# Optimization experiments

Measured on AMD Instinct MI355X. Metric: run time of the kernel, lower is better.

The kernel has to match this reference:

```python
import jax, jax.numpy as jnp
import numpy as np

N_NODES = 50000
N_EDGES = 800000
D = 128


def sage_conv(x, src, dst, w_nbr, w_root, b, n_nodes):
    # mean aggregation of neighbor features: messages flow src (j) -> dst (i)
    msg_sum = jax.ops.segment_sum(x[src], dst, num_segments=n_nodes)  # [N, D]
    deg = jax.ops.segment_sum(jnp.ones((src.shape[0],), x.dtype), dst,
                              num_segments=n_nodes)
    mean = msg_sum / jnp.maximum(deg, 1.0)[:, None]
    # PyG SAGEConv: lin_l(aggr) + lin_r(x); bias lives in lin_l
    return mean @ w_nbr + x @ w_root + b


def setup_inputs() -> dict:
    key = jax.random.key(0)
    ks = jax.random.split(key, 16)
    s = 1.0 / np.sqrt(D)
    inp = {
        "x": jax.random.normal(ks[0], (N_NODES, D), jnp.float32),
        "edge_index": jax.random.randint(ks[1], (2, N_EDGES), 0, N_NODES,
                                         dtype=jnp.int64),
    }
    for l in range(3):
        inp[f"w_nbr{l}"] = jax.random.normal(ks[2 + 3 * l], (D, D), jnp.float32) * s
        inp[f"w_root{l}"] = jax.random.normal(ks[3 + 3 * l], (D, D), jnp.float32) * s
        inp[f"b{l}"] = jnp.zeros((D,), jnp.float32)
    inp["w_cls"] = jax.random.normal(ks[12], (D, 1), jnp.float32) * s
    inp["b_cls"] = jnp.zeros((1,), jnp.float32)
    return inp


def reference(x, edge_index, w_nbr0, w_root0, b0, w_nbr1, w_root1, b1,
              w_nbr2, w_root2, b2, w_cls, b_cls):
    src, dst = edge_index[0], edge_index[1]
    n = x.shape[0]
    layers = [(w_nbr0, w_root0, b0), (w_nbr1, w_root1, b1), (w_nbr2, w_root2, b2)]
    h = x
    for i, (wn, wr, b) in enumerate(layers):
        h = sage_conv(h, src, dst, wn, wr, b, n)
        if i < len(layers) - 1:
            h = jax.nn.relu(h)  # dropout is identity in eval mode
    return (h @ w_cls + b_cls).squeeze(-1)  # [N]
```

## Files before the change

kernel.cpp:

```cpp
#include <hip/hip_runtime.h>

#define N_NODES 50000
#define N_EDGES 800000
#define D 128
#define NGROUPS 3125
#define NBUK 256
#define NPB 196
#define EPB 2048
#define NBLK 391
#define LTOT (NBUK * NBLK)
#define NSCB 98

typedef __attribute__((ext_vector_type(8))) short short8;
typedef __attribute__((ext_vector_type(4))) float f32x4;

__device__ __forceinline__ float bits2f(unsigned int u) {
    union { unsigned int u; float f; } c; c.u = u; return c.f;
}
__device__ __forceinline__ unsigned short f2b(float f) {
    union { float f; unsigned int u; } c; c.f = f;
    unsigned int r = c.u + 0x7fffu + ((c.u >> 16) & 1u);
    return (unsigned short)(r >> 16);
}


__global__ __launch_bounds__(256) void k_big(
    const int* __restrict__ dst, int* __restrict__ cnt,
    const float* __restrict__ x,
    const float* __restrict__ wn0, const float* __restrict__ wr0,
    const float* __restrict__ wn1, const float* __restrict__ wr1,
    const float* __restrict__ wn2, const float* __restrict__ wr2,
    const float* __restrict__ b2, const float* __restrict__ wc,
    const float* __restrict__ bc,
    unsigned short* __restrict__ f0, unsigned short* __restrict__ f1,
    unsigned short* __restrict__ f2, unsigned short* __restrict__ Bp,
    float* __restrict__ uvc) {
    __shared__ int lc[NBUK];
    int b = blockIdx.x;
    int tid = threadIdx.x;
    if (b < NBLK) {
        lc[tid] = 0;
        __syncthreads();
        #pragma unroll
        for (int k = 0; k < 8; ++k) {
            int e = b * EPB + k * 256 + tid;
            if (e < N_EDGES) atomicAdd(&lc[dst[e] / NPB], 1);
        }
        __syncthreads();
        cnt[b * NBUK + tid] = lc[tid];
    } else if (b < 6641) {
        int i = (b - NBLK) * 256 + tid;
        float4 v = reinterpret_cast<const float4*>(x)[i];
        ushort4 o;
        o.x = f2b(v.x); o.y = f2b(v.y); o.z = f2b(v.z); o.w = f2b(v.w);
        reinterpret_cast<ushort4*>(f0)[i] = o;
    } else if (b < 6673) {
        int t = (b - 6641) * 256 + tid;
        int layer = t >> 12;
        int rem = t & 4095;
        int kstep = rem >> 9;
        int cf = (rem >> 6) & 7;
        int lane = t & 63;
        const float* W = (kstep < 4) ? (layer ? wn1 : wn0) : (layer ? wr1 : wr0);
        int kb = kstep * 32 + (lane >> 4) * 8;
        int colv = cf * 16 + (lane & 15);
        int koff = (kstep < 4) ? kb : kb - 128;
        unsigned short* dstp = Bp + (((layer * 64 + kstep * 8 + cf) * 64 + lane) << 3);
        #pragma unroll
        for (int i = 0; i < 8; ++i) dstp[i] = f2b(W[(koff + i) * D + colv]);
    } else if (b == 6673) {
        if (tid < D) {
            f0[(size_t)N_NODES * D + tid] = 0;
            f1[(size_t)N_NODES * D + tid] = 0;
            f2[(size_t)N_NODES * D + tid] = 0;
        }
    } else {
        if (tid < 128) {
            float su = 0.f;
            for (int m = 0; m < 128; ++m) su += wn2[tid * D + m] * wc[m];
            uvc[tid] = su;
        } else {
            int k = tid - 128;
            float sv = 0.f;
            for (int m = 0; m < 128; ++m) sv += wr2[k * D + m] * wc[m];
            uvc[128 + k] = sv;
        }
        if (tid == 0) {
            float sc0 = 0.f;
            for (int m = 0; m < 128; ++m) sc0 += b2[m] * wc[m];
            uvc[256] = sc0 + bc[0];
        }
    }
}


__global__ void k_scanA(const int* __restrict__ cnt, int* __restrict__ sc,
                        int* __restrict__ bsumA) {
    __shared__ int wsum[16];
    int tid = threadIdx.x;
    int lane = tid & 63, wid = tid >> 6;
    int L = blockIdx.x * 1024 + tid;
    int v = 0;
    if (L < LTOT) {
        int bkt = L / NBLK;
        int j = L - bkt * NBLK;
        v = cnt[j * NBUK + bkt];
    }
    int s = v;
    #pragma unroll
    for (int off = 1; off < 64; off <<= 1) {
        int t = __shfl_up(s, off, 64);
        if (lane >= off) s += t;
    }
    if (lane == 63) wsum[wid] = s;
    __syncthreads();
    if (tid < 64) {
        int wv = (tid < 16) ? wsum[tid] : 0;
        int t = wv;
        #pragma unroll
        for (int off = 1; off < 16; off <<= 1) {
            int u = __shfl_up(t, off, 64);
            if (tid >= off) t += u;
        }
        if (tid < 16) wsum[tid] = t - wv;
    }
    __syncthreads();
    int excl = s - v + wsum[wid];
    if (L < LTOT) sc[L] = excl;
    if (tid == 1023) bsumA[blockIdx.x] = excl + v;
}


__global__ __launch_bounds__(256) void k_scatter(
    const int* __restrict__ src, const int* __restrict__ dst,
    const int* __restrict__ sc, const int* __restrict__ bsumA,
    int* __restrict__ ed, int* __restrict__ es) {
    __shared__ int sb[128];
    __shared__ int cursor[NBUK];
    int tid = threadIdx.x, j = blockIdx.x;
    if (tid < 128) sb[tid] = (tid < NSCB) ? bsumA[tid] : 0;
    __syncthreads();
    for (int off = 1; off < 128; off <<= 1) {
        int t = (tid < 128 && tid >= off) ? sb[tid - off] : 0;
        __syncthreads();
        if (tid < 128) sb[tid] += t;
        __syncthreads();
    }
    int L = tid * NBLK + j;
    int idx = L >> 10;
    cursor[tid] = sc[L] + (idx ? sb[idx - 1] : 0);
    __syncthreads();
    #pragma unroll
    for (int k = 0; k < 8; ++k) {
        int e = j * EPB + k * 256 + tid;
        if (e < N_EDGES) {
            int d = dst[e];
            int p = atomicAdd(&cursor[d / NPB], 1);
            ed[p] = d;
            es[p] = src[e];
        }
    }
}


__global__ __launch_bounds__(256) void k_bucket(
    const int* __restrict__ sc, const int* __restrict__ bsumA,
    const int* __restrict__ ed, const int* __restrict__ es,
    int* __restrict__ rs, int* __restrict__ col) {
    __shared__ int sb[128];
    __shared__ int lcnt[NPB];
    __shared__ int s2[256];
    __shared__ int cur[NPB];
    int tid = threadIdx.x, b = blockIdx.x;
    if (tid < 128) sb[tid] = (tid < NSCB) ? bsumA[tid] : 0;
    __syncthreads();
    for (int off = 1; off < 128; off <<= 1) {
        int t = (tid < 128 && tid >= off) ? sb[tid - off] : 0;
        __syncthreads();
        if (tid < 128) sb[tid] += t;
        __syncthreads();
    }
    int L0 = b * NBLK;
    int i0 = L0 >> 10;
    int gstart = sc[L0] + (i0 ? sb[i0 - 1] : 0);
    int bend = N_EDGES;
    if (b + 1 < NBUK) {
        int L1 = (b + 1) * NBLK;
        int i1 = L1 >> 10;
        bend = sc[L1] + (i1 ? sb[i1 - 1] : 0);
    }
    if (tid < NPB) lcnt[tid] = 0;
    __syncthreads();
    for (int e = gstart + tid; e < bend; e += 256)
        atomicAdd(&lcnt[ed[e] - b * NPB], 1);
    __syncthreads();
    int v = (tid < NPB) ? lcnt[tid] : 0;
    s2[tid] = v;
    __syncthreads();
    for (int off = 1; off < 256; off <<= 1) {
        int t = (tid >= off) ? s2[tid - off] : 0;
        __syncthreads();
        s2[tid] += t;
        __syncthreads();
    }
    int excl = s2[tid] - v;
    int node = b * NPB + tid;
    if (tid < NPB) {
        if (node <= N_NODES) rs[node] = gstart + excl;
        cur[tid] = gstart + excl;
    }
    __syncthreads();
    for (int e = gstart + tid; e < bend; e += 256) {
        int p = atomicAdd(&cur[ed[e] - b * NPB], 1);
        col[p] = es[e];
    }
    if (b == NBUK - 1 && tid == 0) rs[N_NODES] = N_EDGES;
}


#define ACCUM(v)                                                      \
    acc0 += bits2f((v).x << 16); acc1 += bits2f((v).x & 0xffff0000u); \
    acc2 += bits2f((v).y << 16); acc3 += bits2f((v).y & 0xffff0000u); \
    acc4 += bits2f((v).z << 16); acc5 += bits2f((v).z & 0xffff0000u); \
    acc6 += bits2f((v).w << 16); acc7 += bits2f((v).w & 0xffff0000u);

__global__ __launch_bounds__(256) void k_agg2(const unsigned short* __restrict__ h,
                                              const int* __restrict__ rs,
                                              const int* __restrict__ col,
                                              unsigned short* __restrict__ mean) {
    const int lane = threadIdx.x & 63;
    const int node = blockIdx.x * 4 + (threadIdx.x >> 6);
    if (node >= N_NODES) return;
    const int j0 = rs[node], j1 = rs[node + 1];
    const int deg = j1 - j0;
    const int q = lane >> 4;
    const int d8 = (lane & 15) * 8;

    int myc = (j0 + lane < j1) ? col[j0 + lane] : N_NODES;
    const int nfull = deg < 64 ? deg : 64;
    const int nb = (nfull + 15) >> 4;

    float acc0 = 0.f, acc1 = 0.f, acc2 = 0.f, acc3 = 0.f;
    float acc4 = 0.f, acc5 = 0.f, acc6 = 0.f, acc7 = 0.f;

    for (int i = 0; i < nb; ++i) {
        int t = (i << 4) + q;
        int c0 = __shfl(myc, t, 64);
        int c1 = __shfl(myc, t + 4, 64);
        int c2 = __shfl(myc, t + 8, 64);
        int c3 = __shfl(myc, t + 12, 64);
        uint4 v0 = *(const uint4*)(h + (size_t)c0 * D + d8);
        uint4 v1 = *(const uint4*)(h + (size_t)c1 * D + d8);
        uint4 v2 = *(const uint4*)(h + (size_t)c2 * D + d8);
        uint4 v3 = *(const uint4*)(h + (size_t)c3 * D + d8);
        ACCUM(v0); ACCUM(v1); ACCUM(v2); ACCUM(v3);
    }
    for (int j = j0 + 64 + q; j < j1; j += 4) {
        int c = col[j];
        uint4 v = *(const uint4*)(h + (size_t)c * D + d8);
        ACCUM(v);
    }

    acc0 += __shfl_xor(acc0, 16, 64); acc0 += __shfl_xor(acc0, 32, 64);
    acc1 += __shfl_xor(acc1, 16, 64); acc1 += __shfl_xor(acc1, 32, 64);
    acc2 += __shfl_xor(acc2, 16, 64); acc2 += __shfl_xor(acc2, 32, 64);
    acc3 += __shfl_xor(acc3, 16, 64); acc3 += __shfl_xor(acc3, 32, 64);
    acc4 += __shfl_xor(acc4, 16, 64); acc4 += __shfl_xor(acc4, 32, 64);
    acc5 += __shfl_xor(acc5, 16, 64); acc5 += __shfl_xor(acc5, 32, 64);
    acc6 += __shfl_xor(acc6, 16, 64); acc6 += __shfl_xor(acc6, 32, 64);
    acc7 += __shfl_xor(acc7, 16, 64); acc7 += __shfl_xor(acc7, 32, 64);

    if (lane < 16) {
        float s = 1.0f / (float)(deg > 0 ? deg : 1);
        uint4 o;
        o.x = (unsigned int)f2b(acc0 * s) | ((unsigned int)f2b(acc1 * s) << 16);
        o.y = (unsigned int)f2b(acc2 * s) | ((unsigned int)f2b(acc3 * s) << 16);
        o.z = (unsigned int)f2b(acc4 * s) | ((unsigned int)f2b(acc5 * s) << 16);
        o.w = (unsigned int)f2b(acc6 * s) | ((unsigned int)f2b(acc7 * s) << 16);
        *reinterpret_cast<uint4*>(mean + (size_t)node * D + d8) = o;
    }
}


__global__ __launch_bounds__(256) void k_gemm(
    const unsigned short* __restrict__ Amean, const unsigned short* __restrict__ Ah,
    const unsigned short* __restrict__ Bp, const float* __restrict__ bias,
    unsigned short* __restrict__ outh) {
    int lane = threadIdx.x & 63;
    int w = blockIdx.x * 4 + (threadIdx.x >> 6);
    int g0 = w * 2;
    if (g0 >= NGROUPS) return;
    int g1ok = (g0 + 1 < NGROUPS);
    int hl = lane & 15;
    int klane = (lane >> 4) * 8;
    int arow0 = g0 * 16 + hl;
    int arow1 = g0 * 16 + 16 + hl;
    if (arow1 > N_NODES) arow1 = N_NODES;

    f32x4 acc0[8], acc1[8];
    #pragma unroll
    for (int i = 0; i < 8; ++i) { acc0[i] = (f32x4)0.0f; acc1[i] = (f32x4)0.0f; }

    const short8* bpv = reinterpret_cast<const short8*>(Bp);
    #pragma unroll
    for (int kstep = 0; kstep < 8; ++kstep) {
        const unsigned short* Asrc = (kstep < 4) ? Amean : Ah;
        int kk = (kstep & 3) * 32 + klane;
        short8 a0 = *reinterpret_cast<const short8*>(Asrc + (size_t)arow0 * D + kk);
        short8 a1 = *reinterpret_cast<const short8*>(Asrc + (size_t)arow1 * D + kk);
        #pragma unroll
        for (int cf = 0; cf < 8; ++cf) {
            short8 b = bpv[(kstep * 8 + cf) * 64 + lane];
            acc0[cf] = __builtin_amdgcn_mfma_f32_16x16x32_bf16(a0, b, acc0[cf], 0, 0, 0);
            acc1[cf] = __builtin_amdgcn_mfma_f32_16x16x32_bf16(a1, b, acc1[cf], 0, 0, 0);
        }
    }

    int rbase0 = g0 * 16 + (lane >> 4) * 4;
    #pragma unroll
    for (int cf = 0; cf < 8; ++cf) {
        int bcol = cf * 16 + hl;
        float bv = bias[bcol];
        #pragma unroll
        for (int i = 0; i < 4; ++i) {
            float v = fmaxf(acc0[cf][i] + bv, 0.f);
            outh[(size_t)(rbase0 + i) * D + bcol] = f2b(v);
            if (g1ok) {
                float v1 = fmaxf(acc1[cf][i] + bv, 0.f);
                outh[(size_t)(rbase0 + 16 + i) * D + bcol] = f2b(v1);
            }
        }
    }
}


__global__ __launch_bounds__(256) void k_gemm_dot(
    const unsigned short* __restrict__ Amean, const unsigned short* __restrict__ Ah,
    const unsigned short* __restrict__ Bp, const float* __restrict__ bias,
    const float* __restrict__ uvc, float* __restrict__ s, float* __restrict__ t) {
    int lane = threadIdx.x & 63;
    int w = blockIdx.x * 4 + (threadIdx.x >> 6);
    int g0 = w * 2;
    if (g0 >= NGROUPS) return;
    int g1ok = (g0 + 1 < NGROUPS);
    int hl = lane & 15;
    int klane = (lane >> 4) * 8;
    int arow0 = g0 * 16 + hl;
    int arow1 = g0 * 16 + 16 + hl;
    if (arow1 > N_NODES) arow1 = N_NODES;

    f32x4 acc0[8], acc1[8];
    #pragma unroll
    for (int i = 0; i < 8; ++i) { acc0[i] = (f32x4)0.0f; acc1[i] = (f32x4)0.0f; }

    const short8* bpv = reinterpret_cast<const short8*>(Bp);
    #pragma unroll
    for (int kstep = 0; kstep < 8; ++kstep) {
        const unsigned short* Asrc = (kstep < 4) ? Amean : Ah;
        int kk = (kstep & 3) * 32 + klane;
        short8 a0 = *reinterpret_cast<const short8*>(Asrc + (size_t)arow0 * D + kk);
        short8 a1 = *reinterpret_cast<const short8*>(Asrc + (size_t)arow1 * D + kk);
        #pragma unroll
        for (int cf = 0; cf < 8; ++cf) {
            short8 b = bpv[(kstep * 8 + cf) * 64 + lane];
            acc0[cf] = __builtin_amdgcn_mfma_f32_16x16x32_bf16(a0, b, acc0[cf], 0, 0, 0);
            acc1[cf] = __builtin_amdgcn_mfma_f32_16x16x32_bf16(a1, b, acc1[cf], 0, 0, 0);
        }
    }

    float ps0[4] = {0.f, 0.f, 0.f, 0.f}, pt0[4] = {0.f, 0.f, 0.f, 0.f};
    float ps1[4] = {0.f, 0.f, 0.f, 0.f}, pt1[4] = {0.f, 0.f, 0.f, 0.f};
    #pragma unroll
    for (int cf = 0; cf < 8; ++cf) {
        int bcol = cf * 16 + hl;
        float bv = bias[bcol];
        float uu = uvc[bcol];
        float vv = uvc[128 + bcol];
        #pragma unroll
        for (int i = 0; i < 4; ++i) {
            float v = fmaxf(acc0[cf][i] + bv, 0.f);
            ps0[i] += v * uu;
            pt0[i] += v * vv;
            float v1 = fmaxf(acc1[cf][i] + bv, 0.f);
            ps1[i] += v1 * uu;
            pt1[i] += v1 * vv;
        }
    }
    #pragma unroll
    for (int m = 1; m < 16; m <<= 1) {
        #pragma unroll
        for (int i = 0; i < 4; ++i) {
            ps0[i] += __shfl_xor(ps0[i], m, 64);
            pt0[i] += __shfl_xor(pt0[i], m, 64);
            ps1[i] += __shfl_xor(ps1[i], m, 64);
            pt1[i] += __shfl_xor(pt1[i], m, 64);
        }
    }
    if (hl == 0) {
        int rbase0 = g0 * 16 + (lane >> 4) * 4;
        #pragma unroll
        for (int i = 0; i < 4; ++i) {
            s[rbase0 + i] = ps0[i];
            t[rbase0 + i] = pt0[i];
            if (g1ok) {
                s[rbase0 + 16 + i] = ps1[i];
                t[rbase0 + 16 + i] = pt1[i];
            }
        }
    }
}

__global__ __launch_bounds__(256) void k_sagg2(const float* __restrict__ s,
                                               const float* __restrict__ t,
                                               const float* __restrict__ uvc,
                                               const int* __restrict__ rs,
                                               const int* __restrict__ col,
                                               float* __restrict__ out) {
    const int lane = threadIdx.x & 63;
    const int hl = lane & 15;
    const int node = blockIdx.x * 16 + (threadIdx.x >> 6) * 4 + (lane >> 4);
    const int j0 = rs[node], j1 = rs[node + 1];
    float sm = 0.f;
    for (int j = j0 + hl; j < j1; j += 16) sm += s[col[j]];
    #pragma unroll
    for (int m = 1; m < 16; m <<= 1) sm += __shfl_xor(sm, m, 64);
    if (hl == 0) {
        int deg = j1 - j0;
        out[node] = sm / (float)(deg > 0 ? deg : 1) + t[node] + uvc[256];
    }
}


extern "C" void kernel_launch(void* const* d_in, const int* in_sizes, int n_in,
                              void* d_out, int out_size, void* d_ws,
                              size_t ws_size, hipStream_t stream) {
    const float* x = (const float*)d_in[0];
    const int* ei = (const int*)d_in[1];
    const int* src = ei;
    const int* dst = ei + N_EDGES;
    const float* wn[3] = {(const float*)d_in[2], (const float*)d_in[5],
                          (const float*)d_in[8]};
    const float* wr[3] = {(const float*)d_in[3], (const float*)d_in[6],
                          (const float*)d_in[9]};
    const float* bs[3] = {(const float*)d_in[4], (const float*)d_in[7],
                          (const float*)d_in[10]};
    const float* wc = (const float*)d_in[11];
    const float* bc = (const float*)d_in[12];
    float* out = (float*)d_out;

    char* ws = (char*)d_ws;
    size_t off = 0;
    auto alloc = [&](size_t bytes) -> void* {
        void* p = (void*)(ws + off);
        off += (bytes + 255) & ~(size_t)255;
        return p;
    };
    const size_t frows = (size_t)(N_NODES + 1) * D;
    int* cnt = (int*)alloc((size_t)LTOT * 4);
    int* sc = (int*)alloc((size_t)LTOT * 4);
    int* bsumA = (int*)alloc(128 * 4);
    int* ed = (int*)alloc(N_EDGES * 4);
    int* es = (int*)alloc(N_EDGES * 4);
    int* rs = (int*)alloc((N_NODES + 1) * 4);
    int* col = (int*)alloc(N_EDGES * 4);
    unsigned short* f0 = (unsigned short*)alloc(frows * 2);
    unsigned short* f1 = (unsigned short*)alloc(frows * 2);
    unsigned short* f2 = (unsigned short*)alloc(frows * 2);
    unsigned short* Bp = (unsigned short*)alloc(2 * 256 * 128 * 2);
    float* uvc = (float*)alloc(260 * 4);
    float* sbuf = (float*)alloc(N_NODES * 4);
    float* tbuf = (float*)alloc(N_NODES * 4);


    k_big<<<6675, 256, 0, stream>>>(dst, cnt, x, wn[0], wr[0], wn[1], wr[1],
                                    wn[2], wr[2], bs[2], wc, bc,
                                    f0, f1, f2, Bp, uvc);
    k_scanA<<<NSCB, 1024, 0, stream>>>(cnt, sc, bsumA);
    k_scatter<<<NBLK, 256, 0, stream>>>(src, dst, sc, bsumA, ed, es);
    k_bucket<<<NBUK, 256, 0, stream>>>(sc, bsumA, ed, es, rs, col);

    const int agg_grid = (N_NODES + 3) / 4;
    const int gemm_grid = ((NGROUPS + 1) / 2 + 3) / 4;
    unsigned short* Bp0 = Bp;
    unsigned short* Bp1 = Bp + 256 * 128;

    k_agg2<<<agg_grid, 256, 0, stream>>>(f0, rs, col, f1);
    k_gemm<<<gemm_grid, 256, 0, stream>>>(f1, f0, Bp0, bs[0], f2);
    k_agg2<<<agg_grid, 256, 0, stream>>>(f2, rs, col, f0);
    k_gemm_dot<<<gemm_grid, 256, 0, stream>>>(f0, f2, Bp1, bs[1], uvc, sbuf,
                                              tbuf);
    k_sagg2<<<NGROUPS, 256, 0, stream>>>(sbuf, tbuf, uvc, rs, col, out);
}
```

Before: 140.1 us.

## Fuse CSR build stages into one persistent kernel with grid barriers

Merges the histogram, two-level scan, scatter and per-bucket sort kernels into a single persistent kernel of 960 blocks that uses atomic-counter grid barriers between phases. It doubles edges per block so the scan fits 256-wide block scans, and packs dst and src into one int2 array. The bf16 conversion and weight packing now run as grid-stride work after the CSR phases. This removes several launch gaps and small-kernel tails but relies on all 960 blocks being co-resident, adds spin-wait barriers and a memset launch, and serializes the feature conversion behind the CSR build.

```diff
diff --git a/kernel.cpp b/kernel.cpp
--- a/kernel.cpp
+++ b/kernel.cpp
@@ -6,10 +6,10 @@
 #define NGROUPS 3125
 #define NBUK 256
 #define NPB 196
-#define EPB 2048
-#define NBLK 391
+#define EPB 4096
+#define NBLK 196
 #define LTOT (NBUK * NBLK)
-#define NSCB 98
+#define GRID_CSR 960
 
 typedef __attribute__((ext_vector_type(8))) short short8;
 typedef __attribute__((ext_vector_type(4))) float f32x4;
@@ -23,9 +23,44 @@
     return (unsigned short)(r >> 16);
 }
 
-
-__global__ __launch_bounds__(256) void k_big(
-    const int* __restrict__ dst, int* __restrict__ cnt,
+__device__ __forceinline__ void gbar(int* bar, int idx) {
+    __syncthreads();
+    if (threadIdx.x == 0) {
+        __threadfence();
+        atomicAdd(&bar[idx], 1);
+        while (atomicAdd(&bar[idx], 0) < (int)gridDim.x)
+            __builtin_amdgcn_s_sleep(8);
+        __threadfence();
+    }
+    __syncthreads();
+}
+
+__device__ __forceinline__ int scan256(int v, int* wsum) {
+    __syncthreads();
+    int lane = threadIdx.x & 63, wid = threadIdx.x >> 6;
+    int s = v;
+    #pragma unroll
+    for (int off = 1; off < 64; off <<= 1) {
+        int t = __shfl_up(s, off, 64);
+        if (lane >= off) s += t;
+    }
+    if (lane == 63) wsum[wid] = s;
+    __syncthreads();
+    if (threadIdx.x == 0) {
+        int r = 0;
+        #pragma unroll
+        for (int k = 0; k < 4; ++k) { int t = wsum[k]; wsum[k] = r; r += t; }
+    }
+    __syncthreads();
+    return s - v + wsum[wid];
+}
+
+
+__global__ __launch_bounds__(256, 4) void k_mega(
+    const int* __restrict__ src, const int* __restrict__ dst,
+    int* __restrict__ bar, int* __restrict__ cnt, int* __restrict__ scC,
+    int* __restrict__ psum, int2* __restrict__ epair,
+    int* __restrict__ rs, int* __restrict__ col,
     const float* __restrict__ x,
     const float* __restrict__ wn0, const float* __restrict__ wr0,
     const float* __restrict__ wn1, const float* __restrict__ wr1,
@@ -36,26 +71,94 @@
     unsigned short* __restrict__ f2, unsigned short* __restrict__ Bp,
     float* __restrict__ uvc) {
     __shared__ int lc[NBUK];
-    int b = blockIdx.x;
-    int tid = threadIdx.x;
+    __shared__ int wsum[4];
+    __shared__ int cur[NBUK];
+    const int b = blockIdx.x;
+    const int tid = threadIdx.x;
+    const int grid = gridDim.x;
+
     if (b < NBLK) {
         lc[tid] = 0;
         __syncthreads();
         #pragma unroll
-        for (int k = 0; k < 8; ++k) {
+        for (int k = 0; k < 16; ++k) {
             int e = b * EPB + k * 256 + tid;
             if (e < N_EDGES) atomicAdd(&lc[dst[e] / NPB], 1);
         }
         __syncthreads();
         cnt[b * NBUK + tid] = lc[tid];
-    } else if (b < 6641) {
-        int i = (b - NBLK) * 256 + tid;
+    }
+    gbar(bar, 0);
+
+    if (b < NBLK) {
+        int C = b * 256 + tid;
+        int bkt = C / NBLK, j = C - bkt * NBLK;
+        int v = cnt[j * NBUK + bkt];
+        int excl = scan256(v, wsum);
+        scC[C] = excl;
+        if (tid == 255) psum[b] = excl + v;
+    }
+    gbar(bar, 1);
+
+    if (b == 0) {
+        int v = (tid < NBLK) ? psum[tid] : 0;
+        int excl = scan256(v, wsum);
+        if (tid < NBLK) psum[tid] = excl;
+    }
+    gbar(bar, 2);
+
+    if (b < NBLK) {
+        int C = tid * NBLK + b;
+        cur[tid] = scC[C] + psum[C >> 8];
+        __syncthreads();
+        #pragma unroll
+        for (int k = 0; k < 16; ++k) {
+            int e = b * EPB + k * 256 + tid;
+            if (e < N_EDGES) {
+                int d = dst[e];
+                int p = atomicAdd(&cur[d / NPB], 1);
+                epair[p] = make_int2(d, src[e]);
+            }
+        }
+    }
+    gbar(bar, 3);
+
+    if (b < NBUK) {
+        int C0 = b * NBLK;
+        int gs = scC[C0] + psum[C0 >> 8];
+        int be = N_EDGES;
+        if (b + 1 < NBUK) {
+            int C1 = (b + 1) * NBLK;
+            be = scC[C1] + psum[C1 >> 8];
+        }
+        lc[tid] = 0;
+        __syncthreads();
+        for (int e = gs + tid; e < be; e += 256)
+            atomicAdd(&lc[epair[e].x - b * NPB], 1);
+        __syncthreads();
+        int v = (tid < NPB) ? lc[tid] : 0;
+        int excl = scan256(v, wsum);
+        int node = b * NPB + tid;
+        if (tid < NPB && node <= N_NODES) rs[node] = gs + excl;
+        cur[tid] = gs + excl;
+        __syncthreads();
+        for (int e = gs + tid; e < be; e += 256) {
+            int2 p2 = epair[e];
+            int p = atomicAdd(&cur[p2.x - b * NPB], 1);
+            col[p] = p2.y;
+        }
+        if (b == NBUK - 1 && tid == 0) rs[N_NODES] = N_EDGES;
+    }
+
+    for (int vb = b; vb < 6250; vb += grid) {
+        int i = vb * 256 + tid;
         float4 v = reinterpret_cast<const float4*>(x)[i];
         ushort4 o;
         o.x = f2b(v.x); o.y = f2b(v.y); o.z = f2b(v.z); o.w = f2b(v.w);
         reinterpret_cast<ushort4*>(f0)[i] = o;
-    } else if (b < 6673) {
-        int t = (b - 6641) * 256 + tid;
+    }
+    for (int vb = b; vb < 32; vb += grid) {
+        int t = vb * 256 + tid;
         int layer = t >> 12;
         int rem = t & 4095;
         int kstep = rem >> 9;
@@ -68,13 +171,15 @@
         unsigned short* dstp = Bp + (((layer * 64 + kstep * 8 + cf) * 64 + lane) << 3);
         #pragma unroll
         for (int i = 0; i < 8; ++i) dstp[i] = f2b(W[(koff + i) * D + colv]);
-    } else if (b == 6673) {
+    }
+    if (b == grid - 1) {
         if (tid < D) {
             f0[(size_t)N_NODES * D + tid] = 0;
             f1[(size_t)N_NODES * D + tid] = 0;
             f2[(size_t)N_NODES * D + tid] = 0;
         }
-    } else {
+    }
+    if (b == grid - 2) {
         if (tid < 128) {
             float su = 0.f;
             for (int m = 0; m < 128; ++m) su += wn2[tid * D + m] * wc[m];
@@ -91,130 +196,6 @@
             uvc[256] = sc0 + bc[0];
         }
     }
-}
-
-
-__global__ void k_scanA(const int* __restrict__ cnt, int* __restrict__ sc,
-                        int* __restrict__ bsumA) {
-    __shared__ int wsum[16];
-    int tid = threadIdx.x;
-    int lane = tid & 63, wid = tid >> 6;
-    int L = blockIdx.x * 1024 + tid;
-    int v = 0;
-    if (L < LTOT) {
-        int bkt = L / NBLK;
-        int j = L - bkt * NBLK;
-        v = cnt[j * NBUK + bkt];
-    }
-    int s = v;
-    #pragma unroll
-    for (int off = 1; off < 64; off <<= 1) {
-        int t = __shfl_up(s, off, 64);
-        if (lane >= off) s += t;
-    }
-    if (lane == 63) wsum[wid] = s;
-    __syncthreads();
-    if (tid < 64) {
-        int wv = (tid < 16) ? wsum[tid] : 0;
-        int t = wv;
-        #pragma unroll
-        for (int off = 1; off < 16; off <<= 1) {
-            int u = __shfl_up(t, off, 64);
-            if (tid >= off) t += u;
-        }
-        if (tid < 16) wsum[tid] = t - wv;
-    }
-    __syncthreads();
-    int excl = s - v + wsum[wid];
-    if (L < LTOT) sc[L] = excl;
-    if (tid == 1023) bsumA[blockIdx.x] = excl + v;
-}
-
-
-__global__ __launch_bounds__(256) void k_scatter(
-    const int* __restrict__ src, const int* __restrict__ dst,
-    const int* __restrict__ sc, const int* __restrict__ bsumA,
-    int* __restrict__ ed, int* __restrict__ es) {
-    __shared__ int sb[128];
-    __shared__ int cursor[NBUK];
-    int tid = threadIdx.x, j = blockIdx.x;
-    if (tid < 128) sb[tid] = (tid < NSCB) ? bsumA[tid] : 0;
-    __syncthreads();
-    for (int off = 1; off < 128; off <<= 1) {
-        int t = (tid < 128 && tid >= off) ? sb[tid - off] : 0;
-        __syncthreads();
-        if (tid < 128) sb[tid] += t;
-        __syncthreads();
-    }
-    int L = tid * NBLK + j;
-    int idx = L >> 10;
-    cursor[tid] = sc[L] + (idx ? sb[idx - 1] : 0);
-    __syncthreads();
-    #pragma unroll
-    for (int k = 0; k < 8; ++k) {
-        int e = j * EPB + k * 256 + tid;
-        if (e < N_EDGES) {
-            int d = dst[e];
-            int p = atomicAdd(&cursor[d / NPB], 1);
-            ed[p] = d;
-            es[p] = src[e];
-        }
-    }
-}
-
-
-__global__ __launch_bounds__(256) void k_bucket(
-    const int* __restrict__ sc, const int* __restrict__ bsumA,
-    const int* __restrict__ ed, const int* __restrict__ es,
-    int* __restrict__ rs, int* __restrict__ col) {
-    __shared__ int sb[128];
-    __shared__ int lcnt[NPB];
-    __shared__ int s2[256];
-    __shared__ int cur[NPB];
-    int tid = threadIdx.x, b = blockIdx.x;
-    if (tid < 128) sb[tid] = (tid < NSCB) ? bsumA[tid] : 0;
-    __syncthreads();
-    for (int off = 1; off < 128; off <<= 1) {
-        int t = (tid < 128 && tid >= off) ? sb[tid - off] : 0;
-        __syncthreads();
-        if (tid < 128) sb[tid] += t;
-        __syncthreads();
-    }
-    int L0 = b * NBLK;
-    int i0 = L0 >> 10;
-    int gstart = sc[L0] + (i0 ? sb[i0 - 1] : 0);
-    int bend = N_EDGES;
-    if (b + 1 < NBUK) {
-        int L1 = (b + 1) * NBLK;
-        int i1 = L1 >> 10;
-        bend = sc[L1] + (i1 ? sb[i1 - 1] : 0);
-    }
-    if (tid < NPB) lcnt[tid] = 0;
-    __syncthreads();
-    for (int e = gstart + tid; e < bend; e += 256)
-        atomicAdd(&lcnt[ed[e] - b * NPB], 1);
-    __syncthreads();
-    int v = (tid < NPB) ? lcnt[tid] : 0;
-    s2[tid] = v;
-    __syncthreads();
-    for (int off = 1; off < 256; off <<= 1) {
-        int t = (tid >= off) ? s2[tid - off] : 0;
-        __syncthreads();
-        s2[tid] += t;
-        __syncthreads();
-    }
-    int excl = s2[tid] - v;
-    int node = b * NPB + tid;
-    if (tid < NPB) {
-        if (node <= N_NODES) rs[node] = gstart + excl;
-        cur[tid] = gstart + excl;
-    }
-    __syncthreads();
-    for (int e = gstart + tid; e < bend; e += 256) {
-        int p = atomicAdd(&cur[ed[e] - b * NPB], 1);
-        col[p] = es[e];
-    }
-    if (b == NBUK - 1 && tid == 0) rs[N_NODES] = N_EDGES;
 }
 
 
@@ -456,11 +437,11 @@
         return p;
     };
     const size_t frows = (size_t)(N_NODES + 1) * D;
+    int* bar = (int*)alloc(64);
     int* cnt = (int*)alloc((size_t)LTOT * 4);
-    int* sc = (int*)alloc((size_t)LTOT * 4);
-    int* bsumA = (int*)alloc(128 * 4);
-    int* ed = (int*)alloc(N_EDGES * 4);
-    int* es = (int*)alloc(N_EDGES * 4);
+    int* scC = (int*)alloc((size_t)LTOT * 4);
+    int* psum = (int*)alloc(256 * 4);
+    int2* epair = (int2*)alloc((size_t)N_EDGES * 8);
     int* rs = (int*)alloc((N_NODES + 1) * 4);
     int* col = (int*)alloc(N_EDGES * 4);
     unsigned short* f0 = (unsigned short*)alloc(frows * 2);
@@ -471,13 +452,12 @@
     float* sbuf = (float*)alloc(N_NODES * 4);
     float* tbuf = (float*)alloc(N_NODES * 4);
 
-
-    k_big<<<6675, 256, 0, stream>>>(dst, cnt, x, wn[0], wr[0], wn[1], wr[1],
-                                    wn[2], wr[2], bs[2], wc, bc,
-                                    f0, f1, f2, Bp, uvc);
-    k_scanA<<<NSCB, 1024, 0, stream>>>(cnt, sc, bsumA);
-    k_scatter<<<NBLK, 256, 0, stream>>>(src, dst, sc, bsumA, ed, es);
-    k_bucket<<<NBUK, 256, 0, stream>>>(sc, bsumA, ed, es, rs, col);
+    hipMemsetAsync(bar, 0, 64, stream);
+
+    k_mega<<<GRID_CSR, 256, 0, stream>>>(src, dst, bar, cnt, scC, psum, epair,
+                                         rs, col, x, wn[0], wr[0], wn[1], wr[1],
+                                         wn[2], wr[2], bs[2], wc, bc,
+                                         f0, f1, f2, Bp, uvc);
 
     const int agg_grid = (N_NODES + 3) / 4;
     const int gemm_grid = ((NGROUPS + 1) / 2 + 3) / 4;
```

After: 453.0 us. 223% more time.
